# Performance work log

Measured on AMD Instinct MI355X. Metric: run time of the kernel, lower is better.

The kernel has to match this reference:

```python
import jax, jax.numpy as jnp
import numpy as np

HIDDEN = 2048
NUM_HEADS = 16
HEAD = HIDDEN // NUM_HEADS  # 128
B, S = 4, 2048  # equal-length prefill sequences (cu_seqlens = arange(B+1)*S)


def setup_inputs() -> dict:
    key = jax.random.key(0)
    ks = jax.random.split(key, 5)
    return {
        "hidden_states": jax.random.normal(ks[0], (B * S, HIDDEN), jnp.float32),
        # fused QKV weight: rows ordered [q(all heads), k(all heads), v(all heads)]
        "w_qkv": jax.random.normal(ks[1], (3 * HIDDEN, HIDDEN), jnp.float32) * 0.02,
        "b_qkv": jax.random.normal(ks[2], (3 * HIDDEN,), jnp.float32) * 0.02,
        "w_dense": jax.random.normal(ks[3], (HIDDEN, HIDDEN), jnp.float32) * 0.02,
        "b_dense": jax.random.normal(ks[4], (HIDDEN,), jnp.float32) * 0.02,
        "batch_size": B,
        "seq_len": S,
    }


def reference(hidden_states, w_qkv, b_qkv, w_dense, b_dense, batch_size, seq_len):
    # QKV projection: [T, hidden] -> [T, 3, H, D]
    qkv = hidden_states @ w_qkv.T + b_qkv
    qkv = qkv.reshape(batch_size, seq_len, 3, NUM_HEADS, HEAD)
    q, k, v = qkv[:, :, 0], qkv[:, :, 1], qkv[:, :, 2]  # each [B, S, H, D]

    softmax_scale = HEAD ** -0.5
    # varlen causal flash attention (prefill path), per-sequence causal mask
    scores = jnp.einsum("bqhd,bkhd->bhqk", q, k) * softmax_scale
    causal = jnp.tril(jnp.ones((seq_len, seq_len), dtype=bool))
    scores = jnp.where(causal, scores, jnp.finfo(scores.dtype).min)
    probs = jax.nn.softmax(scores, axis=-1)
    attn = jnp.einsum("bhqk,bkhd->bqhd", probs, v)  # [B, S, H, D]

    attn = attn.reshape(batch_size * seq_len, NUM_HEADS * HEAD)
    # output projection (resid dropout p=0 -> identity)
    return attn @ w_dense.T + b_dense
```

## Files before the change

### kernel.cpp

```cpp
#include <hip/hip_runtime.h>
#include <hip/hip_bf16.h>

#define HIDDEN 2048
#define NHEADS 16
#define HEADD  128
#define BATCH  4
#define SEQ    2048
#define MROWS  (BATCH*SEQ)
#define NQKV   (3*HIDDEN)

typedef __attribute__((ext_vector_type(8))) short bf16x8;
typedef __attribute__((ext_vector_type(4))) float f32x4;

__device__ inline unsigned short f2bf(float f) {
  unsigned int u = __builtin_bit_cast(unsigned int, f);
  u += 0x7FFF + ((u >> 16) & 1);
  return (unsigned short)(u >> 16);
}

__device__ inline void async16(const void* g, void* s) {
  __builtin_amdgcn_global_load_lds(
      (__attribute__((address_space(1))) void*)(g),
      (__attribute__((address_space(3))) void*)(s), 16, 0, 0);
}

#define PH_BAR() asm volatile("s_barrier" ::: "memory")
#define LGKM0()  asm volatile("s_waitcnt lgkmcnt(0)" ::: "memory")
#define VMC6()   asm volatile("s_waitcnt vmcnt(6)" ::: "memory")
#define VMC0()   asm volatile("s_waitcnt vmcnt(0)" ::: "memory")

__global__ __launch_bounds__(256)
void cvt_f32_bf16(const float* __restrict__ in, unsigned short* __restrict__ out, int n) {
  int i = (blockIdx.x * 256 + threadIdx.x) * 8;
  if (i + 8 <= n) {
    float4 a = *(const float4*)&in[i];
    float4 b = *(const float4*)&in[i + 4];
    unsigned short o[8];
    o[0] = f2bf(a.x); o[1] = f2bf(a.y); o[2] = f2bf(a.z); o[3] = f2bf(a.w);
    o[4] = f2bf(b.x); o[5] = f2bf(b.y); o[6] = f2bf(b.z); o[7] = f2bf(b.w);
    *(uint4*)&out[i] = *(uint4*)o;
  }
}


#define MFMA_QUAD(AB, NB, AF, BF)                                           \
  _Pragma("unroll")                                                         \
  for (int mi = 0; mi < 4; ++mi)                                            \
    _Pragma("unroll")                                                       \
    for (int e = 0; e < 2; ++e)                                             \
      _Pragma("unroll")                                                     \
      for (int ks = 0; ks < 2; ++ks)                                        \
        acc[(AB) + mi][(NB) + e] = __builtin_amdgcn_mfma_f32_16x16x32_bf16( \
            AF[mi][ks], BF[e][ks], acc[(AB) + mi][(NB) + e], 0, 0, 0);

#define RD_A(DST, BUF, H)                                                   \
  _Pragma("unroll")                                                         \
  for (int mi = 0; mi < 4; ++mi) {                                          \
    DST[mi][0] = rdA(BUF, H, mi, 0);                                        \
    DST[mi][1] = rdA(BUF, H, mi, 1);                                        \
  }

#define RD_B(DST, BUF, H)                                                   \
  _Pragma("unroll")                                                         \
  for (int e = 0; e < 2; ++e) {                                             \
    DST[e][0] = rdB(BUF, H, e, 0);                                          \
    DST[e][1] = rdB(BUF, H, e, 1);                                          \
  }

template<int OUT_BF16>
__global__ __launch_bounds__(512, 2)
void gemm256(const unsigned short* __restrict__ A,
             const unsigned short* __restrict__ Bw,
             const float* __restrict__ bias,
             void* __restrict__ Cout, int M, int N, int K) {
  __shared__ __align__(16) unsigned short L[2][2][2][8192];

  const int t = threadIdx.x;
  const int lane = t & 63, wv = t >> 6;
  const int r = lane & 15, q = lane >> 4;
  const int wm = wv >> 2, wn = wv & 3;
  const int r7 = r & 7;

  const int gx = gridDim.x;
  const int nwg = gx * (int)gridDim.y;
  const int id = (int)blockIdx.y * gx + (int)blockIdx.x;
  const int swz = (id & 7) * (nwg >> 3) + (id >> 3);
  const int m0 = (swz / gx) * 256;
  const int n0 = (swz % gx) * 256;

  const int sub = t >> 3;
  const int cb = (t & 7) ^ (sub & 7);
  unsigned offA[2][2], offB[2][2];
#pragma unroll
  for (int ld = 0; ld < 2; ++ld) {
    int row = ld * 64 + sub;
    int fs = row >> 4, r16 = row & 15;
    int gA = (fs & 3) | ((fs >> 2) << 3);
    int gB = (fs & 1) | ((fs >> 1) << 2);
#pragma unroll
    for (int h = 0; h < 2; ++h) {
      offA[h][ld] = (unsigned)(m0 + (gA | (h << 2)) * 16 + r16) * (unsigned)K + cb * 8;
      offB[h][ld] = (unsigned)(n0 + (gB | (h << 1)) * 16 + r16) * (unsigned)K + cb * 8;
    }
  }

  auto stgA = [&](int buf, int h, int tile) {
    async16(A + (size_t)(offA[h][0] + (unsigned)tile * 64), &L[buf][0][h][t * 8]);
    async16(A + (size_t)(offA[h][1] + (unsigned)tile * 64), &L[buf][0][h][4096 + t * 8]);
  };
  auto stgB = [&](int buf, int h, int tile) {
    async16(Bw + (size_t)(offB[h][0] + (unsigned)tile * 64), &L[buf][1][h][t * 8]);
    async16(Bw + (size_t)(offB[h][1] + (unsigned)tile * 64), &L[buf][1][h][4096 + t * 8]);
  };
  auto rdA = [&](int buf, int h, int mi, int ks) -> bf16x8 {
    int row = (wm * 4 + mi) * 16 + r;
    int c = (ks * 4 + q) ^ r7;
    return *(const bf16x8*)&L[buf][0][h][row * 64 + c * 8];
  };
  auto rdB = [&](int buf, int h, int e, int ks) -> bf16x8 {
    int row = (wn * 2 + e) * 16 + r;
    int c = (ks * 4 + q) ^ r7;
    return *(const bf16x8*)&L[buf][1][h][row * 64 + c * 8];
  };

  f32x4 acc[8][4] = {};
  bf16x8 a0[4][2], a1[4][2], b0[2][2], b1[2][2];

  stgA(0, 0, 0); stgB(0, 0, 0); stgA(0, 1, 0); stgB(0, 1, 0);
  stgA(1, 0, 1); stgB(1, 0, 1); stgA(1, 1, 1);
  VMC6(); PH_BAR();

  const int NT = K >> 6;
  const int NITER = K >> 7;
#pragma unroll 1
  for (int i = 0; i < NITER; ++i) {
    const int ta = 2 * i + 1;
    int tb = 2 * i + 2; if (tb > NT - 1) tb = NT - 1;
    int tc = 2 * i + 3; if (tc > NT - 1) tc = NT - 1;

    RD_A(a0, 0, 0); RD_B(b0, 0, 0);
    stgB(1, 1, ta);
    PH_BAR(); LGKM0(); __builtin_amdgcn_s_setprio(1);
    MFMA_QUAD(0, 0, a0, b0);
    __builtin_amdgcn_s_setprio(0); PH_BAR();

    RD_A(a1, 0, 1);
    stgA(0, 0, tb);
    PH_BAR(); LGKM0(); __builtin_amdgcn_s_setprio(1);
    MFMA_QUAD(4, 0, a1, b0);
    __builtin_amdgcn_s_setprio(0); PH_BAR();

    RD_B(b1, 0, 1);
    stgB(0, 0, tb);
    PH_BAR(); LGKM0(); __builtin_amdgcn_s_setprio(1);
    MFMA_QUAD(4, 2, a1, b1);
    __builtin_amdgcn_s_setprio(0); PH_BAR();

    stgA(0, 1, tb);
    PH_BAR(); LGKM0(); __builtin_amdgcn_s_setprio(1);
    MFMA_QUAD(0, 2, a0, b1);
    __builtin_amdgcn_s_setprio(0); VMC6(); PH_BAR();

    RD_A(a0, 1, 0); RD_B(b0, 1, 0);
    stgB(0, 1, tb);
    PH_BAR(); LGKM0(); __builtin_amdgcn_s_setprio(1);
    MFMA_QUAD(0, 0, a0, b0);
    __builtin_amdgcn_s_setprio(0); PH_BAR();

    RD_A(a1, 1, 1);
    stgA(1, 0, tc);
    PH_BAR(); LGKM0(); __builtin_amdgcn_s_setprio(1);
    MFMA_QUAD(4, 0, a1, b0);
    __builtin_amdgcn_s_setprio(0); PH_BAR();

    RD_B(b1, 1, 1);
    stgB(1, 0, tc);
    PH_BAR(); LGKM0(); __builtin_amdgcn_s_setprio(1);
    MFMA_QUAD(4, 2, a1, b1);
    __builtin_amdgcn_s_setprio(0); PH_BAR();

    stgA(1, 1, tc);
    PH_BAR(); LGKM0(); __builtin_amdgcn_s_setprio(1);
    MFMA_QUAD(0, 2, a0, b1);
    __builtin_amdgcn_s_setprio(0); VMC6(); PH_BAR();
  }
  VMC0();

  float bv[4];
#pragma unroll
  for (int ni = 0; ni < 4; ++ni) bv[ni] = bias[n0 + (wn * 4 + ni) * 16 + r];
#pragma unroll
  for (int ai = 0; ai < 8; ++ai) {
    int grow = m0 + (wm * 8 + ai) * 16 + q * 4;
#pragma unroll
    for (int ni = 0; ni < 4; ++ni) {
      int gcol = n0 + (wn * 4 + ni) * 16 + r;
#pragma unroll
      for (int rr = 0; rr < 4; ++rr) {
        float v = acc[ai][ni][rr] + bv[ni];
        if (OUT_BF16)
          ((unsigned short*)Cout)[(size_t)(grow + rr) * N + gcol] = f2bf(v);
        else
          ((float*)Cout)[(size_t)(grow + rr) * N + gcol] = v;
      }
    }
  }
}

__global__ __launch_bounds__(256, 2)
void flash_attn(const unsigned short* __restrict__ qkv,
                unsigned short* __restrict__ attn)
{
  __shared__ __align__(16) unsigned short Ks[64][128];
  __shared__ __align__(16) unsigned short Vt[128][64];
  __shared__ __align__(16) unsigned short Ps[4][32][64];

  const int t = threadIdx.x;
  const int lane = t & 63, wv = t >> 6;
  const int r = lane & 15, q = lane >> 4;
  const int b = blockIdx.y >> 4, h = blockIdx.y & 15;
  const int qt = (int)(gridDim.x - 1 - blockIdx.x);
  const int q0 = qt * 128;

  const size_t rs = NQKV;
  const unsigned short* qbase = qkv + (size_t)(b * SEQ) * rs + h * HEADD;
  const unsigned short* kbase = qbase + HIDDEN;
  const unsigned short* vbase = qbase + 2 * HIDDEN;

  bf16x8 qf[2][4];
  for (int i = 0; i < 2; ++i)
    for (int ks = 0; ks < 4; ++ks)
      qf[i][ks] = *(const bf16x8*)(qbase +
          (size_t)(q0 + wv * 32 + i * 16 + r) * rs + ks * 32 + q * 8);

  f32x4 accO[2][8] = {};
  float lsum[2][4] = {};

  const int ntiles = 2 * qt + 2;
  const int diag0 = 2 * qt;
  const float sc2 = 0.08838834764831845f * 1.4426950408889634f;

  const int koct = t & 15, krb = t >> 4;
  const int bd4 = t & 15, bkv4 = t >> 4;

  uint4 kreg[4], vreg[4];
  for (int s = 0; s < 4; ++s)
    kreg[s] = *(const uint4*)(kbase + (size_t)(krb + 16 * s) * rs + koct * 8);
  for (int jr = 0; jr < 4; ++jr)
    vreg[jr] = *(const uint4*)(vbase + (size_t)(bkv4 * 4 + jr) * rs + bd4 * 8);

  for (int tk = 0; tk < ntiles; ++tk) {
    __syncthreads();
    for (int s = 0; s < 4; ++s) {
      int row = krb + 16 * s;
      int cbk = koct ^ (row & 7);
      *(uint4*)&Ks[row][cbk * 8] = kreg[s];
    }
    for (int jj = 0; jj < 8; ++jj) {
      int d = bd4 * 8 + jj;
      int cbk = (bkv4 >> 1) ^ jj ^ (bd4 & 7);
      unsigned short tmp[4];
      for (int jr = 0; jr < 4; ++jr)
        tmp[jr] = ((const unsigned short*)&vreg[jr])[jj];
      *(uint2*)&Vt[d][cbk * 8 + (bkv4 & 1) * 4] = *(const uint2*)tmp;
    }
    __syncthreads();
    if (tk + 1 < ntiles) {
      for (int s = 0; s < 4; ++s)
        kreg[s] = *(const uint4*)(kbase + (size_t)((tk + 1) * 64 + krb + 16 * s) * rs + koct * 8);
      for (int jr = 0; jr < 4; ++jr)
        vreg[jr] = *(const uint4*)(vbase + (size_t)((tk + 1) * 64 + bkv4 * 4 + jr) * rs + bd4 * 8);
    }

    f32x4 s[2][4] = {};
    for (int ks = 0; ks < 4; ++ks) {
      bf16x8 bk[4];
      for (int j = 0; j < 4; ++j) {
        int row = j * 16 + r;
        int cbk = (ks * 4 + q) ^ (r & 7);
        bk[j] = *(const bf16x8*)&Ks[row][cbk * 8];
      }
      for (int i = 0; i < 2; ++i)
        for (int j = 0; j < 4; ++j)
          s[i][j] = __builtin_amdgcn_mfma_f32_16x16x32_bf16(qf[i][ks], bk[j], s[i][j], 0, 0, 0);
    }

    const bool diag = (tk >= diag0);
    for (int i = 0; i < 2; ++i) {
      float pvv[4][4];
      for (int j = 0; j < 4; ++j)
        for (int rr = 0; rr < 4; ++rr) {
          float v = s[i][j][rr] * sc2;
          if (diag) {
            int kvp = tk * 64 + j * 16 + r;
            int qp = q0 + wv * 32 + i * 16 + q * 4 + rr;
            if (kvp > qp) v = -1e30f;
          }
          float p = __builtin_amdgcn_exp2f(v);
          pvv[j][rr] = p;
          lsum[i][rr] += p;
        }
      for (int j = 0; j < 4; ++j)
        for (int rr = 0; rr < 4; ++rr) {
          int m = i * 16 + q * 4 + rr;
          int k = j * 16 + r;
          int cbk = (k >> 3) ^ (m & 7);
          Ps[wv][m][cbk * 8 + (k & 7)] = f2bf(pvv[j][rr]);
        }
    }

    for (int ks2 = 0; ks2 < 2; ++ks2) {
      bf16x8 ap[2];
      for (int i = 0; i < 2; ++i) {
        int m = i * 16 + r;
        int cbk = (ks2 * 4 + q) ^ (r & 7);
        ap[i] = *(const bf16x8*)&Ps[wv][m][cbk * 8];
      }
      for (int n = 0; n < 8; ++n) {
        int dd = n * 16 + r;
        int cbk = (ks2 * 4 + q) ^ (r & 7) ^ ((n * 2 + (r >> 3)) & 7);
        bf16x8 bvv = *(const bf16x8*)&Vt[dd][cbk * 8];
        for (int i = 0; i < 2; ++i)
          accO[i][n] = __builtin_amdgcn_mfma_f32_16x16x32_bf16(ap[i], bvv, accO[i][n], 0, 0, 0);
      }
    }
  }

  for (int i = 0; i < 2; ++i)
    for (int rr = 0; rr < 4; ++rr) {
      float l = lsum[i][rr];
      for (int off = 1; off < 16; off <<= 1)
        l += __shfl_xor(l, off, 64);
      lsum[i][rr] = l;
    }
  for (int i = 0; i < 2; ++i)
    for (int rr = 0; rr < 4; ++rr) {
      int row = q0 + wv * 32 + i * 16 + q * 4 + rr;
      float inv = 1.0f / lsum[i][rr];
      size_t obase = (size_t)(b * SEQ + row) * HIDDEN + h * HEADD;
      for (int n = 0; n < 8; ++n)
        attn[obase + n * 16 + r] = f2bf(accO[i][n][rr] * inv);
    }
}

extern "C" void kernel_launch(void* const* d_in, const int* in_sizes, int n_in,
                              void* d_out, int out_size, void* d_ws, size_t ws_size,
                              hipStream_t stream) {
  const float* hs      = (const float*)d_in[0];
  const float* w_qkv   = (const float*)d_in[1];
  const float* b_qkv   = (const float*)d_in[2];
  const float* w_dense = (const float*)d_in[3];
  const float* b_dense = (const float*)d_in[4];

  char* ws = (char*)d_ws;
  unsigned short* hsb  = (unsigned short*)ws;
  unsigned short* wqb  = (unsigned short*)(ws + 33554432);
  unsigned short* qkvb = (unsigned short*)(ws + 33554432 + 25165824);
  unsigned short* attnb = hsb;
  unsigned short* wdb   = wqb;

  cvt_f32_bf16<<<MROWS * HIDDEN / 2048, 256, 0, stream>>>(hs, hsb, MROWS * HIDDEN);
  cvt_f32_bf16<<<NQKV * HIDDEN / 2048, 256, 0, stream>>>(w_qkv, wqb, NQKV * HIDDEN);

  gemm256<1><<<dim3(NQKV / 256, MROWS / 256), 512, 0, stream>>>(
      hsb, wqb, b_qkv, qkvb, MROWS, NQKV, HIDDEN);

  flash_attn<<<dim3(SEQ / 128, BATCH * NHEADS), 256, 0, stream>>>(qkvb, attnb);

  cvt_f32_bf16<<<HIDDEN * HIDDEN / 2048, 256, 0, stream>>>(w_dense, wdb, HIDDEN * HIDDEN);

  gemm256<0><<<dim3(HIDDEN / 256, MROWS / 256), 512, 0, stream>>>(
      attnb, wdb, b_dense, d_out, MROWS, HIDDEN, HIDDEN);
}
```

Measured before the change: 634.2 us.

## Split long causal query tiles across KV chunks with atomic fp32 reduction

```diff
diff --git a/kernel.cpp b/kernel.cpp
--- a/kernel.cpp
+++ b/kernel.cpp
@@ -41,7 +41,6 @@
     *(uint4*)&out[i] = *(uint4*)o;
   }
 }
-
 
 #define MFMA_QUAD(AB, NB, AF, BF)                                           \
   _Pragma("unroll")                                                         \
@@ -207,20 +206,28 @@
   }
 }
 
-__global__ __launch_bounds__(256, 2)
+__global__ __launch_bounds__(256, 4)
 void flash_attn(const unsigned short* __restrict__ qkv,
-                unsigned short* __restrict__ attn)
+                unsigned short* __restrict__ attn,
+                float* __restrict__ outF,
+                float* __restrict__ lsumB)
 {
   __shared__ __align__(16) unsigned short Ks[64][128];
   __shared__ __align__(16) unsigned short Vt[128][64];
-  __shared__ __align__(16) unsigned short Ps[4][32][64];
 
   const int t = threadIdx.x;
   const int lane = t & 63, wv = t >> 6;
   const int r = lane & 15, q = lane >> 4;
   const int b = blockIdx.y >> 4, h = blockIdx.y & 15;
-  const int qt = (int)(gridDim.x - 1 - blockIdx.x);
+
+  int f = (int)blockIdx.x, qt, c;
+  if (f < 16) { qt = 15 - (f >> 1); c = f & 1; }
+  else        { qt = 23 - f;        c = 0; }
   const int q0 = qt * 128;
+  const int t0 = c * 16;
+  int t1 = 2 * qt + 2; if (t1 > t0 + 16) t1 = t0 + 16;
+
+  unsigned short* Ps = &Ks[0][0] + wv * 2048;
 
   const size_t rs = NQKV;
   const unsigned short* qbase = qkv + (size_t)(b * SEQ) * rs + h * HEADD;
@@ -236,7 +243,6 @@
   f32x4 accO[2][8] = {};
   float lsum[2][4] = {};
 
-  const int ntiles = 2 * qt + 2;
   const int diag0 = 2 * qt;
   const float sc2 = 0.08838834764831845f * 1.4426950408889634f;
 
@@ -245,11 +251,11 @@
 
   uint4 kreg[4], vreg[4];
   for (int s = 0; s < 4; ++s)
-    kreg[s] = *(const uint4*)(kbase + (size_t)(krb + 16 * s) * rs + koct * 8);
+    kreg[s] = *(const uint4*)(kbase + (size_t)(t0 * 64 + krb + 16 * s) * rs + koct * 8);
   for (int jr = 0; jr < 4; ++jr)
-    vreg[jr] = *(const uint4*)(vbase + (size_t)(bkv4 * 4 + jr) * rs + bd4 * 8);
-
-  for (int tk = 0; tk < ntiles; ++tk) {
+    vreg[jr] = *(const uint4*)(vbase + (size_t)(t0 * 64 + bkv4 * 4 + jr) * rs + bd4 * 8);
+
+  for (int tk = t0; tk < t1; ++tk) {
     __syncthreads();
     for (int s = 0; s < 4; ++s) {
       int row = krb + 16 * s;
@@ -265,7 +271,7 @@
       *(uint2*)&Vt[d][cbk * 8 + (bkv4 & 1) * 4] = *(const uint2*)tmp;
     }
     __syncthreads();
-    if (tk + 1 < ntiles) {
+    if (tk + 1 < t1) {
       for (int s = 0; s < 4; ++s)
         kreg[s] = *(const uint4*)(kbase + (size_t)((tk + 1) * 64 + krb + 16 * s) * rs + koct * 8);
       for (int jr = 0; jr < 4; ++jr)
@@ -273,6 +279,7 @@
     }
 
     f32x4 s[2][4] = {};
+    __builtin_amdgcn_s_setprio(1);
     for (int ks = 0; ks < 4; ++ks) {
       bf16x8 bk[4];
       for (int j = 0; j < 4; ++j) {
@@ -284,6 +291,8 @@
         for (int j = 0; j < 4; ++j)
           s[i][j] = __builtin_amdgcn_mfma_f32_16x16x32_bf16(qf[i][ks], bk[j], s[i][j], 0, 0, 0);
     }
+    __builtin_amdgcn_s_setprio(0);
+    __syncthreads();
 
     const bool diag = (tk >= diag0);
     for (int i = 0; i < 2; ++i) {
@@ -305,16 +314,17 @@
           int m = i * 16 + q * 4 + rr;
           int k = j * 16 + r;
           int cbk = (k >> 3) ^ (m & 7);
-          Ps[wv][m][cbk * 8 + (k & 7)] = f2bf(pvv[j][rr]);
+          Ps[m * 64 + cbk * 8 + (k & 7)] = f2bf(pvv[j][rr]);
         }
     }
 
+    __builtin_amdgcn_s_setprio(1);
     for (int ks2 = 0; ks2 < 2; ++ks2) {
       bf16x8 ap[2];
       for (int i = 0; i < 2; ++i) {
         int m = i * 16 + r;
         int cbk = (ks2 * 4 + q) ^ (r & 7);
-        ap[i] = *(const bf16x8*)&Ps[wv][m][cbk * 8];
+        ap[i] = *(const bf16x8*)&Ps[m * 64 + cbk * 8];
       }
       for (int n = 0; n < 8; ++n) {
         int dd = n * 16 + r;
@@ -324,6 +334,7 @@
           accO[i][n] = __builtin_amdgcn_mfma_f32_16x16x32_bf16(ap[i], bvv, accO[i][n], 0, 0, 0);
       }
     }
+    __builtin_amdgcn_s_setprio(0);
   }
 
   for (int i = 0; i < 2; ++i)
@@ -333,14 +344,47 @@
         l += __shfl_xor(l, off, 64);
       lsum[i][rr] = l;
     }
-  for (int i = 0; i < 2; ++i)
-    for (int rr = 0; rr < 4; ++rr) {
-      int row = q0 + wv * 32 + i * 16 + q * 4 + rr;
-      float inv = 1.0f / lsum[i][rr];
-      size_t obase = (size_t)(b * SEQ + row) * HIDDEN + h * HEADD;
-      for (int n = 0; n < 8; ++n)
-        attn[obase + n * 16 + r] = f2bf(accO[i][n][rr] * inv);
-    }
+
+  if (qt < 8) {
+    for (int i = 0; i < 2; ++i)
+      for (int rr = 0; rr < 4; ++rr) {
+        int row = q0 + wv * 32 + i * 16 + q * 4 + rr;
+        float inv = 1.0f / lsum[i][rr];
+        size_t obase = (size_t)(b * SEQ + row) * HIDDEN + h * HEADD;
+        for (int n = 0; n < 8; ++n)
+          attn[obase + n * 16 + r] = f2bf(accO[i][n][rr] * inv);
+      }
+  } else {
+    for (int i = 0; i < 2; ++i)
+      for (int rr = 0; rr < 4; ++rr) {
+        int row = q0 + wv * 32 + i * 16 + q * 4 + rr;
+        if (r == 0)
+          unsafeAtomicAdd(&lsumB[(size_t)((b << 10) + row - 1024) * 16 + h], lsum[i][rr]);
+        size_t obase = (size_t)(b * SEQ + row) * HIDDEN + h * HEADD;
+        for (int n = 0; n < 8; ++n)
+          unsafeAtomicAdd(&outF[obase + n * 16 + r], accO[i][n][rr]);
+      }
+  }
+}
+
+__global__ __launch_bounds__(256)
+void attn_norm(const float* __restrict__ outF, const float* __restrict__ lsumB,
+               unsigned short* __restrict__ attn) {
+  int j = (blockIdx.x * 256 + threadIdx.x) * 8;
+  int b = j >> 21;
+  int rl = (j >> 11) & 1023;
+  int col = j & 2047;
+  int h = col >> 7;
+  float inv = 1.0f / lsumB[(size_t)((b << 10) + rl) * 16 + h];
+  size_t base = (size_t)((b << 11) + 1024 + rl) * 2048 + col;
+  float4 a = *(const float4*)&outF[base];
+  float4 c4 = *(const float4*)&outF[base + 4];
+  unsigned short o[8];
+  o[0] = f2bf(a.x * inv);  o[1] = f2bf(a.y * inv);
+  o[2] = f2bf(a.z * inv);  o[3] = f2bf(a.w * inv);
+  o[4] = f2bf(c4.x * inv); o[5] = f2bf(c4.y * inv);
+  o[6] = f2bf(c4.z * inv); o[7] = f2bf(c4.w * inv);
+  *(uint4*)&attn[base] = *(uint4*)o;
 }
 
 extern "C" void kernel_launch(void* const* d_in, const int* in_sizes, int n_in,
@@ -358,6 +402,8 @@
   unsigned short* qkvb = (unsigned short*)(ws + 33554432 + 25165824);
   unsigned short* attnb = hsb;
   unsigned short* wdb   = wqb;
+  float* lsumB = (float*)(ws + 33554432 + 16777216);
+  float* outF  = (float*)d_out;
 
   cvt_f32_bf16<<<MROWS * HIDDEN / 2048, 256, 0, stream>>>(hs, hsb, MROWS * HIDDEN);
   cvt_f32_bf16<<<NQKV * HIDDEN / 2048, 256, 0, stream>>>(w_qkv, wqb, NQKV * HIDDEN);
@@ -365,9 +411,16 @@
   gemm256<1><<<dim3(NQKV / 256, MROWS / 256), 512, 0, stream>>>(
       hsb, wqb, b_qkv, qkvb, MROWS, NQKV, HIDDEN);
 
-  flash_attn<<<dim3(SEQ / 128, BATCH * NHEADS), 256, 0, stream>>>(qkvb, attnb);
+  for (int b = 0; b < 4; ++b)
+    hipMemsetAsync((char*)d_out + (size_t)(b * 2048 + 1024) * 2048 * 4, 0,
+                   (size_t)1024 * 2048 * 4, stream);
+  hipMemsetAsync(lsumB, 0, (size_t)4 * 1024 * 16 * 4, stream);
+
+  flash_attn<<<dim3(24, BATCH * NHEADS), 256, 0, stream>>>(qkvb, attnb, outF, lsumB);
 
   cvt_f32_bf16<<<HIDDEN * HIDDEN / 2048, 256, 0, stream>>>(w_dense, wdb, HIDDEN * HIDDEN);
+
+  attn_norm<<<4096, 256, 0, stream>>>(outF, lsumB, attnb);
 
   gemm256<0><<<dim3(HIDDEN / 256, MROWS / 256), 512, 0, stream>>>(
       attnb, wdb, b_dense, d_out, MROWS, HIDDEN, HIDDEN);
```

New measurement: 1.346 ms. 112% more time.
